# Kernel tuning notes

Hardware: AMD Instinct MI355X
Metric: run time of the kernel (lower is better)

Reference implementation:

```python
import jax, jax.numpy as jnp
import numpy as np

CHUNK = 32
HEADS = 4
EPS_RMS = 1e-5

def silu(x):
    return jax.nn.silu(x)

def l2norm(x, eps=1e-6):
    return x * jax.lax.rsqrt(jnp.sum(x * x, axis=-1, keepdims=True) + eps)

def short_conv(x, w):
    # x: (b, l, c); w: (c, K) depthwise causal conv, no bias
    K = w.shape[1]
    L = x.shape[1]
    xp = jnp.pad(x, ((0, 0), (K - 1, 0), (0, 0)))
    out = xp[:, 0:L, :] * w[:, 0]
    for k in range(1, K):
        out = out + xp[:, k:k + L, :] * w[:, k]
    return out

def delta_rule_chunkwise(q, k, v, beta, chunk=CHUNK):
    # q,k: (b,h,l,dk); v: (b,h,l,dv); beta: (b,h,l). l divisible by chunk.
    b, h, l, dk = q.shape
    dv = v.shape[-1]
    n = l // chunk
    q = l2norm(q)
    k = l2norm(k)
    v = v * beta[..., None]
    k_beta = k * beta[..., None]
    resh = lambda x: x.reshape(b, h, n, chunk, -1)
    q, k, v, k_beta = map(resh, (q, k, v, k_beta))
    strict_lower = jnp.tril(jnp.ones((chunk, chunk), bool), -1)
    # A = -(k_beta k^T) kept strictly lower triangular
    attn = jnp.where(strict_lower, -(k_beta @ jnp.swapaxes(k, -1, -2)), 0.0)
    # forward substitution: T = (I - A)^{-1} - I built row by row (fixed 32 rows)
    for i in range(1, chunk):
        row = attn[..., i, :]                                  # (b,h,n,c)
        new = attn[..., i, :i] + jnp.einsum('...j,...jk->...k', row, attn[..., :, :i])
        attn = attn.at[..., i, :i].set(new)
    attn = attn + jnp.eye(chunk, dtype=attn.dtype)
    u = attn @ v        # (b,h,n,c,dv)
    w = attn @ k_beta   # (b,h,n,c,dk)
    lower_incl = jnp.tril(jnp.ones((chunk, chunk), bool))
    qc, kc, uc, wc = [jnp.moveaxis(x, 2, 0) for x in (q, k, u, w)]
    S0 = jnp.zeros((b, h, dk, dv), q.dtype)
    def step(S, inp):
        q_i, k_i, u_i, w_i = inp
        attn_i = jnp.where(lower_incl, q_i @ jnp.swapaxes(k_i, -1, -2), 0.0)
        u_adj = u_i - w_i @ S
        o_i = q_i @ S + attn_i @ u_adj
        S = S + jnp.swapaxes(k_i, -1, -2) @ u_adj
        return S, o_i
    S, o = jax.lax.scan(step, S0, (qc, kc, uc, wc))
    o = jnp.moveaxis(o, 0, 2).reshape(b, h, l, dv)
    return o, S

def ema_rule(v, gamma):
    # v: (b,h,l,dv), gamma: (b,h,l); sequential EMA scan
    v_t = jnp.moveaxis(v, 2, 0)       # (l,b,h,dv)
    g_t = jnp.moveaxis(gamma, 2, 0)   # (l,b,h)
    s0 = jnp.zeros(v.shape[:2] + (v.shape[-1],), v.dtype)
    def step(s, inp):
        vt, gt = inp
        s = gt[..., None] * s + (1.0 - gt[..., None]) * vt
        return s, s
    s_fin, out = jax.lax.scan(step, s0, (v_t, g_t))
    return jnp.moveaxis(out, 0, 2), s_fin

def rms_norm(x, w, eps=EPS_RMS):
    return x * jax.lax.rsqrt(jnp.mean(x * x, axis=-1, keepdims=True) + eps) * w

def setup_inputs() -> dict:
    key = jax.random.key(0)
    ks = jax.random.split(key, 16)
    b, l, d = 4, 2048, 1024
    H, conv_K = HEADS, 4
    s = 0.02
    return {
        'hidden_states': jax.random.normal(ks[0], (b, l, d), jnp.float32),
        'Wq': jax.random.normal(ks[1], (d, d), jnp.float32) * s,
        'Wk': jax.random.normal(ks[2], (d, d), jnp.float32) * s,
        'Wv': jax.random.normal(ks[3], (d, d), jnp.float32) * s,
        'conv_q': jax.random.normal(ks[4], (d, conv_K), jnp.float32) * 0.3,
        'conv_k': jax.random.normal(ks[5], (d, conv_K), jnp.float32) * 0.3,
        'conv_v': jax.random.normal(ks[6], (d, conv_K), jnp.float32) * 0.3,
        'Wb': jax.random.normal(ks[7], (d, H), jnp.float32) * s,
        'Wdec': jax.random.normal(ks[8], (d, H), jnp.float32) * s,
        'Wmix': jax.random.normal(ks[9], (d, H), jnp.float32) * s,
        'conv_mix': jax.random.normal(ks[10], (H, conv_K), jnp.float32) * 0.3,
        'mix_bias': jnp.full((H,), -2.0, jnp.float32),
        'rms_w': jnp.ones((d // H,), jnp.float32),
        'Wo': jax.random.normal(ks[11], (d, d), jnp.float32) * s,
    }

def reference(hidden_states, Wq, Wk, Wv, conv_q, conv_k, conv_v, Wb, Wdec, Wmix, conv_mix, mix_bias, rms_w, Wo):
    b, l, d = hidden_states.shape
    H = HEADS
    dk = d // H
    dv = d // H
    # projections + causal depthwise short conv (silu activation inside conv)
    q = silu(short_conv(hidden_states @ Wq, conv_q))
    k = silu(short_conv(hidden_states @ Wk, conv_k))
    v = silu(short_conv(hidden_states @ Wv, conv_v))
    mix_inp = silu(short_conv(hidden_states @ Wmix, conv_mix))  # (b,l,H)
    # qk_activation == 'silu' applies an extra silu after conv (per source)
    q = silu(q)
    k = silu(k)
    # split heads -> (b,H,l,dh)
    to_heads = lambda x, dh: jnp.transpose(x.reshape(b, l, H, dh), (0, 2, 1, 3))
    q_d = to_heads(q, dk)
    k_d = to_heads(k, dk)
    v_d = to_heads(v, dv)
    beta = jax.nn.sigmoid(hidden_states @ Wb)           # (b,l,H)
    beta_d = jnp.transpose(beta, (0, 2, 1))             # (b,H,l)
    o_d, S = delta_rule_chunkwise(q_d, k_d, v_d, beta_d)
    o_d = jnp.transpose(o_d, (0, 2, 1, 3))              # (b,l,H,dv)
    # EMA branch
    gamma = jax.nn.sigmoid(hidden_states @ Wdec)        # (b,l,H)
    gamma_d = jnp.transpose(gamma, (0, 2, 1))
    ema_out, ema_state = ema_rule(v_d, gamma_d)
    ema_out = jnp.transpose(ema_out, (0, 2, 1, 3))      # (b,l,H,dv)
    # fine-grained head mix gate
    mix = jax.nn.sigmoid(mix_inp + mix_bias)            # (b,l,H)
    o = (1.0 - mix[..., None]) * o_d + mix[..., None] * ema_out
    # per-head RMSNorm then output projection
    o = rms_norm(o, rms_w)
    out = o.reshape(b, l, H * dv) @ Wo
    return out
```

## Files before the change

### kernel.cpp

```cpp
#include <hip/hip_runtime.h>
#include <hip/hip_bf16.h>

#define B 4
#define L 2048
#define D 1024
#define NH 4
#define DK 256
#define CHUNK 32
#define NCH 64
#define BH (B*NH)
#define ET 64
#define ENCH (L/ET)

typedef __attribute__((ext_vector_type(8))) __bf16 bf16x8;
typedef __attribute__((ext_vector_type(4))) __bf16 bf16x4;
typedef __attribute__((ext_vector_type(4))) float f32x4;

__device__ inline unsigned short f2bf(float f) {
    union { float f; unsigned u; } v; v.f = f;
    unsigned r = v.u + 0x7fffu + ((v.u >> 16) & 1u);
    return (unsigned short)(r >> 16);
}
__device__ inline float bf2f(unsigned short h) {
    union { unsigned u; float f; } v; v.u = ((unsigned)h) << 16; return v.f;
}
__device__ inline float sigmoidf_(float x) { return 1.0f / (1.0f + __expf(-x)); }
__device__ inline float siluf_(float x) { return x / (1.0f + __expf(-x)); }

#define MFMA16(a, b, c) __builtin_amdgcn_mfma_f32_16x16x32_bf16((a), (b), (c), 0, 0, 0)

__device__ inline void bar_lds() {
    __builtin_amdgcn_s_waitcnt(0xC07F);
    __builtin_amdgcn_s_barrier();
}

__device__ inline void load_lds16(const unsigned short* g, unsigned short* l) {
    __builtin_amdgcn_global_load_lds(
        (const __attribute__((address_space(1))) unsigned int*)g,
        (__attribute__((address_space(3))) unsigned int*)l, 16, 0, 0);
}

__global__ __launch_bounds__(256) void k_wT(const float* Wq, const float* Wk, const float* Wv,
                                            const float* Wo, unsigned short* wT)
{
    __shared__ float tile[32][33];
    int z = blockIdx.z;
    const float* W = (z == 0) ? Wq : (z == 1) ? Wk : (z == 2) ? Wv : Wo;
    unsigned short* out = wT + (size_t)z * D * D;
    int kt = blockIdx.x * 32, nt = blockIdx.y * 32;
    int tx = threadIdx.x & 31, ty = threadIdx.x >> 5;
#pragma unroll
    for (int i = 0; i < 4; i++)
        tile[ty + 8 * i][tx] = W[(size_t)(kt + ty + 8 * i) * D + nt + tx];
    __syncthreads();
#pragma unroll
    for (int i = 0; i < 4; i++)
        out[(size_t)(nt + ty + 8 * i) * D + kt + tx] = f2bf(tile[tx][ty + 8 * i]);
}

__global__ __launch_bounds__(256) void k_cvt(const float* h, unsigned short* hb, int n4)
{
    int i = blockIdx.x * blockDim.x + threadIdx.x;
    int stride = gridDim.x * blockDim.x;
    const float4* h4 = (const float4*)h;
    for (; i < n4; i += stride) {
        float4 v = h4[i];
        ushort4 o;
        o.x = f2bf(v.x); o.y = f2bf(v.y); o.z = f2bf(v.z); o.w = f2bf(v.w);
        *(ushort4*)(hb + 4 * (size_t)i) = o;
    }
}

template<int NTOT, bool OUT_F32>
__global__ __launch_bounds__(256) void k_gemm_lds(const unsigned short* __restrict__ A,
                                                  const unsigned short* __restrict__ BT,
                                                  void* __restrict__ outp)
{
    __shared__ __align__(16) unsigned short As[128 * 32];
    __shared__ __align__(16) unsigned short Bs[128 * 32];
    const int K = 1024;
    int tid = threadIdx.x;
    int w = tid >> 6, lane = tid & 63;
    int r16 = lane & 15, quad = lane >> 4;
    int wm = w & 1, wn = w >> 1;
    int bm = blockIdx.x * 128;
    int bn = blockIdx.y * 128;
    int lrow = lane >> 2;
    int lcol = (lane & 3) * 8;
    f32x4 z4 = {0.f, 0.f, 0.f, 0.f};
    f32x4 acc[4][4];
#pragma unroll
    for (int i = 0; i < 4; i++)
#pragma unroll
        for (int j = 0; j < 4; j++) acc[i][j] = z4;

    for (int kt = 0; kt < K; kt += 32) {
#pragma unroll
        for (int j = 0; j < 2; j++) {
            int r0 = (w * 2 + j) * 16;
            load_lds16(A + (size_t)(bm + r0 + lrow) * K + kt + lcol, &As[r0 * 32]);
            load_lds16(BT + (size_t)(bn + r0 + lrow) * K + kt + lcol, &Bs[r0 * 32]);
        }
        __syncthreads();
        bf16x8 af[4], bf[4];
#pragma unroll
        for (int ms = 0; ms < 4; ms++)
            af[ms] = *(const bf16x8*)&As[(wm * 64 + ms * 16 + r16) * 32 + quad * 8];
#pragma unroll
        for (int ns = 0; ns < 4; ns++)
            bf[ns] = *(const bf16x8*)&Bs[(wn * 64 + ns * 16 + r16) * 32 + quad * 8];
#pragma unroll
        for (int ms = 0; ms < 4; ms++)
#pragma unroll
            for (int ns = 0; ns < 4; ns++)
                acc[ms][ns] = MFMA16(af[ms], bf[ns], acc[ms][ns]);
        __syncthreads();
    }
#pragma unroll
    for (int ms = 0; ms < 4; ms++)
#pragma unroll
        for (int ns = 0; ns < 4; ns++)
#pragma unroll
            for (int r = 0; r < 4; r++) {
                int m = bm + wm * 64 + ms * 16 + quad * 4 + r;
                int n = bn + wn * 64 + ns * 16 + r16;
                if (OUT_F32)
                    ((float*)outp)[(size_t)m * NTOT + n] = acc[ms][ns][r];
                else
                    ((unsigned short*)outp)[(size_t)m * NTOT + n] = f2bf(acc[ms][ns][r]);
            }
}

__global__ __launch_bounds__(256) void k_smallproj(const float* hid, const float* Wb, const float* Wd,
                                                   const float* Wm, float* beta, float* gamma, float* xmix)
{
    int wave = threadIdx.x >> 6, lane = threadIdx.x & 63;
    int row = blockIdx.x * 4 + wave;
    const float* hrow = hid + (size_t)row * D;
    float acc[12];
#pragma unroll
    for (int j = 0; j < 12; j++) acc[j] = 0.f;
    for (int i = 0; i < 16; i++) {
        int k = lane + 64 * i;
        float h = hrow[k];
        float4 wb = ((const float4*)Wb)[k];
        float4 wd = ((const float4*)Wd)[k];
        float4 wm = ((const float4*)Wm)[k];
        acc[0] += h * wb.x; acc[1] += h * wb.y; acc[2] += h * wb.z; acc[3] += h * wb.w;
        acc[4] += h * wd.x; acc[5] += h * wd.y; acc[6] += h * wd.z; acc[7] += h * wd.w;
        acc[8] += h * wm.x; acc[9] += h * wm.y; acc[10] += h * wm.z; acc[11] += h * wm.w;
    }
#pragma unroll
    for (int j = 0; j < 12; j++)
        for (int off = 32; off; off >>= 1) acc[j] += __shfl_xor(acc[j], off, 64);
    if (lane < 4) {
        beta[(size_t)row * 4 + lane] = sigmoidf_(acc[lane]);
        gamma[(size_t)row * 4 + lane] = sigmoidf_(acc[4 + lane]);
        xmix[(size_t)row * 4 + lane] = acc[8 + lane];
    }
}

__global__ __launch_bounds__(256) void k_conv(const unsigned short* xqkv,
                                              const float* cq, const float* ck, const float* cv,
                                              float* q, float* k, float* v)
{
    int z = blockIdx.z;
    const float* cw = (z == 0) ? cq : (z == 1) ? ck : cv;
    float* dst = (z == 0) ? q : (z == 1) ? k : v;
    int idx = blockIdx.x * 256 + threadIdx.x;
    int c = idx & (D - 1);
    int t = (idx >> 10) & (L - 1);
    int b = idx >> 21;
    float4 w4 = *(const float4*)(cw + (size_t)c * 4);
    float wv[4] = {w4.x, w4.y, w4.z, w4.w};
    size_t base = ((size_t)(b * L)) * (3 * D) + z * D + c;
    float acc = 0.f;
#pragma unroll
    for (int kk = 0; kk < 4; kk++) {
        int tt = t - 3 + kk;
        if (tt >= 0) acc += wv[kk] * bf2f(xqkv[base + (size_t)tt * (3 * D)]);
    }
    float r = siluf_(acc);
    if (z < 2) r = siluf_(r);
    dst[idx] = r;
}

__global__ __launch_bounds__(256) void k_convmix(const float* xmix, const float* cmix, float* mixinp)
{
    int idx = blockIdx.x * 256 + threadIdx.x;
    int h = idx & 3;
    int t = (idx >> 2) & (L - 1);
    int b = idx >> 13;
    float acc = 0.f;
#pragma unroll
    for (int kk = 0; kk < 4; kk++) {
        int tt = t - 3 + kk;
        if (tt >= 0) acc += cmix[h * 4 + kk] * xmix[((size_t)(b * L + tt) << 2) + h];
    }
    mixinp[idx] = siluf_(acc);
}

__global__ __launch_bounds__(256) void k_l2norm(const float* qbuf, const float* kbuf,
                                                unsigned short* qn, unsigned short* kn)
{
    int wave = threadIdx.x >> 6, lane = threadIdx.x & 63;
    int rid = blockIdx.x * 4 + wave;
    int bh = rid >> 11, t = rid & (L - 1);
    int b = bh >> 2, h = bh & 3;
    size_t src = (size_t)(b * L + t) * D + h * DK + lane * 4;
    float4 q4 = *(const float4*)(qbuf + src);
    float4 k4 = *(const float4*)(kbuf + src);
    float sq = q4.x * q4.x + q4.y * q4.y + q4.z * q4.z + q4.w * q4.w;
    float sk = k4.x * k4.x + k4.y * k4.y + k4.z * k4.z + k4.w * k4.w;
    for (int off = 32; off; off >>= 1) { sq += __shfl_xor(sq, off, 64); sk += __shfl_xor(sk, off, 64); }
    float qsc = rsqrtf(sq + 1e-6f);
    float ksc = rsqrtf(sk + 1e-6f);
    uint2 pq, pk;
    pq.x = f2bf(q4.x * qsc) | ((unsigned)f2bf(q4.y * qsc) << 16);
    pq.y = f2bf(q4.z * qsc) | ((unsigned)f2bf(q4.w * qsc) << 16);
    pk.x = f2bf(k4.x * ksc) | ((unsigned)f2bf(k4.y * ksc) << 16);
    pk.y = f2bf(k4.z * ksc) | ((unsigned)f2bf(k4.w * ksc) << 16);
    *(uint2*)(qn + (size_t)rid * DK + lane * 4) = pq;
    *(uint2*)(kn + (size_t)rid * DK + lane * 4) = pk;
}

#define KTS 40
__global__ __launch_bounds__(256) void k_delta_pre(const unsigned short* qn, const unsigned short* kn,
                                                   const float* vbuf, const float* beta,
                                                   unsigned short* wneg, unsigned short* knT,
                                                   unsigned short* attnb, float* u)
{
    __shared__ __align__(16) unsigned short kTl[256 * KTS];
    __shared__ __align__(16) unsigned short vTl[256 * KTS];
    __shared__ __align__(16) unsigned short T2b[32 * KTS];
    __shared__ float Gs[32 * 33];
    int bx = blockIdx.x;
    int bh = bx >> 6, ch = bx & 63;
    int b = bh >> 2, h = bh & 3;
    int t0 = ch * 32;
    int tid = threadIdx.x;
    int w = tid >> 6, lane = tid & 63;
    int r16 = lane & 15, quad = lane >> 4;
    size_t rowbase = (size_t)(bh * L + t0);
    f32x4 z4 = {0.f, 0.f, 0.f, 0.f};

    if (w < 3) {
        int mi = (w == 0) ? 0 : 1;
        int ni = (w == 2) ? 1 : 0;
        const unsigned short* krm = kn + (rowbase + mi * 16 + r16) * DK;
        const unsigned short* krn = kn + (rowbase + ni * 16 + r16) * DK;
        const unsigned short* qrm = qn + (rowbase + mi * 16 + r16) * DK;
        f32x4 g = z4, qk = z4;
#pragma unroll
        for (int kt = 0; kt < 8; kt++) {
            bf16x8 a  = *(const bf16x8*)(krm + kt * 32 + quad * 8);
            bf16x8 bb = *(const bf16x8*)(krn + kt * 32 + quad * 8);
            bf16x8 qa = *(const bf16x8*)(qrm + kt * 32 + quad * 8);
            g  = MFMA16(a, bb, g);
            qk = MFMA16(qa, bb, qk);
        }
#pragma unroll
        for (int r = 0; r < 4; r++) {
            int i = mi * 16 + quad * 4 + r, j = ni * 16 + r16;
            Gs[i * 33 + j] = g[r];
            attnb[(size_t)(bh * 64 + ch) * 1024 + i * 32 + j] =
                (j <= i) ? f2bf(qk[r]) : (unsigned short)0;
        }
    } else {
#pragma unroll
        for (int r = 0; r < 4; r++) {
            int i = quad * 4 + r, j = 16 + r16;
            attnb[(size_t)(bh * 64 + ch) * 1024 + i * 32 + j] = 0;
        }
    }
    {
        int t = tid & 31, c0 = (tid >> 5) * 32;
        const unsigned short* krow = kn + (rowbase + t) * DK + c0;
        const float* vrow = vbuf + ((size_t)(b * L + t0 + t)) * D + h * DK + c0;
#pragma unroll
        for (int j = 0; j < 32; j += 4) {
            ushort4 kv = *(const ushort4*)(krow + j);
            float4 vv = *(const float4*)(vrow + j);
            kTl[(c0 + j + 0) * KTS + t] = kv.x;
            kTl[(c0 + j + 1) * KTS + t] = kv.y;
            kTl[(c0 + j + 2) * KTS + t] = kv.z;
            kTl[(c0 + j + 3) * KTS + t] = kv.w;
            vTl[(c0 + j + 0) * KTS + t] = f2bf(vv.x);
            vTl[(c0 + j + 1) * KTS + t] = f2bf(vv.y);
            vTl[(c0 + j + 2) * KTS + t] = f2bf(vv.z);
            vTl[(c0 + j + 3) * KTS + t] = f2bf(vv.w);
        }
    }
    __syncthreads();

    if (w == 0) {
        int c = lane & 31;
        float rr[32];
#pragma unroll
        for (int j = 0; j < 32; j++) rr[j] = Gs[j * 33 + c];
        rr[0] = 0.f;
        float bc = beta[(size_t)(b * L + t0 + c) * NH + h];
#pragma unroll
        for (int i = 1; i < 32; i++) {
            float bi = __shfl(bc, i, 64);
            float s = -bi * rr[i];
#pragma unroll
            for (int j = 1; j < i; j++) {
                float aij = -bi * __shfl(rr[i], j, 64);
                s += aij * ((c < j) ? rr[j] : 0.f);
            }
            rr[i] = (c < i) ? s : 0.f;
        }
        if (lane < 32) {
#pragma unroll
            for (int i = 0; i < 32; i++) {
                float val = (rr[i] + ((i == c) ? 1.f : 0.f)) * bc;
                T2b[i * KTS + c] = f2bf(val);
            }
        }
    } else {
        int idx = tid - 64;
        for (int rowc = idx; rowc < 256; rowc += 192) {
            unsigned short* kT = knT + ((size_t)(bh * 64 + ch) * DK + rowc) * 32;
#pragma unroll
            for (int seg = 0; seg < 4; seg++) {
                uint4 d = *(const uint4*)&kTl[rowc * KTS + seg * 8];
                *(uint4*)(kT + seg * 8) = d;
            }
        }
    }
    __syncthreads();

#pragma unroll
    for (int mt = 0; mt < 2; mt++) {
        bf16x8 ta = *(const bf16x8*)&T2b[(mt * 16 + r16) * KTS + quad * 8];
#pragma unroll
        for (int nt2 = 0; nt2 < 4; nt2++) {
            int nt = w * 4 + nt2;
            bf16x8 vb = *(const bf16x8*)&vTl[(nt * 16 + r16) * KTS + quad * 8];
            bf16x8 kb = *(const bf16x8*)&kTl[(nt * 16 + r16) * KTS + quad * 8];
            f32x4 uu = MFMA16(ta, vb, z4);
            f32x4 ww = MFMA16(ta, kb, z4);
            float* ug = u + (rowbase + mt * 16 + quad * 4) * DK + nt * 16 + r16;
            unsigned short* wg = wneg + (rowbase + mt * 16 + quad * 4) * DK + nt * 16 + r16;
#pragma unroll
            for (int r = 0; r < 4; r++) {
                ug[(size_t)r * DK] = uu[r];
                wg[(size_t)r * DK] = f2bf(-ww[r]);
            }
        }
    }
}

__global__ __launch_bounds__(256) void k_ema_local(const float* v, const float* gamma,
                                                   float* ema_local, float* Acum,
                                                   float* s_end, float* Pchunk)
{
    __shared__ float gsh[ET];
    int blk = blockIdx.x;
    int bh = blk >> 5;
    int ch = blk & (ENCH - 1);
    int b = bh >> 2, h = bh & 3;
    int c = threadIdx.x;
    int t0 = ch * ET;
    if (c < ET) gsh[c] = gamma[(size_t)(b * L + t0 + c) * NH + h];
    __syncthreads();
    const float* vg = v + (size_t)(b * L + t0) * D + h * DK + c;
    float* eg = ema_local + (size_t)(b * L + t0) * D + h * DK + c;
    float* Ag = Acum + (size_t)bh * L + t0;
    float s = 0.f;
    float A = 1.f;
#pragma unroll 8
    for (int i = 0; i < ET; i++) {
        float g = gsh[i];
        s = g * s + (1.f - g) * vg[(size_t)i * D];
        A *= g;
        eg[(size_t)i * D] = s;
        if (c == 0) Ag[i] = A;
    }
    s_end[((size_t)bh * ENCH + ch) * DK + c] = s;
    if (c == 0) Pchunk[(size_t)bh * ENCH + ch] = A;
}

__global__ __launch_bounds__(256) void k_ema_carry(const float* s_end, const float* Pchunk, float* S_in)
{
    int bh = blockIdx.x;
    int c = threadIdx.x;
    float S = 0.f;
    for (int ch = 0; ch < ENCH; ch++) {
        S_in[((size_t)bh * ENCH + ch) * DK + c] = S;
        float P = Pchunk[(size_t)bh * ENCH + ch];
        S = P * S + s_end[((size_t)bh * ENCH + ch) * DK + c];
    }
}

#define STS 280
#define USTR 40
__global__ __launch_bounds__(128, 1) void k_scan(const unsigned short* qn, const unsigned short* wneg,
                                                 const unsigned short* knT, const unsigned short* attnb,
                                                 const float* u, float* od)
{
    __shared__ __align__(16) unsigned short st[16 * STS];
    __shared__ __align__(16) unsigned short uat[16 * USTR];
    int bh = blockIdx.x;
    int tile = blockIdx.y;
    int b = bh >> 2, h = bh & 3;
    int mo = threadIdx.x >> 6, lane = threadIdx.x & 63;
    int r16 = lane & 15, quad = lane >> 4;
    int cbase = tile * 16;
    f32x4 z4 = {0.f, 0.f, 0.f, 0.f};
    f32x4 sacc[8];
#pragma unroll
    for (int a = 0; a < 8; a++) sacc[a] = z4;
    const unsigned short* qb = qn + (size_t)bh * L * DK;
    const unsigned short* wb = wneg + (size_t)bh * L * DK;
    const float* ub = u + (size_t)bh * L * DK;
    const unsigned short* kTbase = knT + (size_t)bh * 64 * DK * 32;
    const unsigned short* atbase = attnb + (size_t)bh * 64 * 1024;
    int dkb = mo * 128;

    bf16x8 qf[2][8], wf[2][8];
    f32x4 au0[2];

    auto issue = [&](int ch, int par) {
        int t0 = ch * 32;
        const unsigned short* wrow = wb + (size_t)(t0 + 16 * mo + r16) * DK;
        const unsigned short* qrow = qb + (size_t)(t0 + 16 * mo + r16) * DK;
#pragma unroll
        for (int kt = 0; kt < 8; kt++) {
            qf[par][kt] = *(const bf16x8*)(qrow + kt * 32 + quad * 8);
            wf[par][kt] = *(const bf16x8*)(wrow + kt * 32 + quad * 8);
        }
        const float* up = ub + (size_t)(t0 + 16 * mo + quad * 4) * DK + cbase + r16;
        f32x4 a; a[0] = up[0]; a[1] = up[DK]; a[2] = up[2 * DK]; a[3] = up[3 * DK];
        au0[par] = a;
    };

    issue(0, 0);

    auto body = [&](int ch, int par) {
        int t0 = ch * 32;
        bf16x8 af = *(const bf16x8*)(atbase + (size_t)ch * 1024 + (16 * mo + r16) * 32 + quad * 8);
        const unsigned short* kTb = kTbase + (size_t)ch * DK * 32;
        bf16x8 kf[8];
#pragma unroll
        for (int a = 0; a < 8; a++)
            kf[a] = *(const bf16x8*)(kTb + (size_t)(dkb + a * 16 + r16) * 32 + quad * 8);

#pragma unroll
        for (int a = 0; a < 8; a++) {
            uint2 p;
            p.x = f2bf(sacc[a][0]) | ((unsigned)f2bf(sacc[a][1]) << 16);
            p.y = f2bf(sacc[a][2]) | ((unsigned)f2bf(sacc[a][3]) << 16);
            *(uint2*)&st[r16 * STS + dkb + a * 16 + quad * 4] = p;
        }
        if (ch + 1 < NCH) issue(ch + 1, par ^ 1);
        bar_lds();

        f32x4 au = au0[par], ao = z4;
#pragma unroll
        for (int kt = 0; kt < 8; kt++) {
            bf16x8 sfr = *(const bf16x8*)&st[r16 * STS + kt * 32 + quad * 8];
            au = MFMA16(wf[par][kt], sfr, au);
            ao = MFMA16(qf[par][kt], sfr, ao);
        }
        {
            uint2 p;
            p.x = f2bf(au[0]) | ((unsigned)f2bf(au[1]) << 16);
            p.y = f2bf(au[2]) | ((unsigned)f2bf(au[3]) << 16);
            *(uint2*)&uat[r16 * USTR + 16 * mo + quad * 4] = p;
        }
        bar_lds();

        {
            bf16x8 uf = *(const bf16x8*)&uat[r16 * USTR + quad * 8];
            ao = MFMA16(af, uf, ao);
            float* op = od + (size_t)(b * L + t0 + 16 * mo + quad * 4) * D + h * DK + cbase + r16;
            op[0] = ao[0]; op[D] = ao[1]; op[2 * D] = ao[2]; op[3 * D] = ao[3];
#pragma unroll
            for (int a = 0; a < 8; a++)
                sacc[a] = MFMA16(kf[a], uf, sacc[a]);
        }
    };

    for (int ch2 = 0; ch2 < NCH; ch2 += 2) {
        body(ch2, 0);
        body(ch2 + 1, 1);
    }
}

__global__ __launch_bounds__(256) void k_mixrms(const float* od, const float* ema_local,
                                                const float* Acum, const float* S_in,
                                                const float* mixinp,
                                                const float* mix_bias, const float* rms_w,
                                                unsigned short* onorm)
{
    int row = blockIdx.x;
    int tid = threadIdx.x;
    int h = tid >> 6, lane = tid & 63;
    int b = row >> 11, t = row & (L - 1);
    int bh = b * NH + h;
    int ch = t >> 6;
    float m = sigmoidf_(mixinp[(size_t)row * NH + h] + mix_bias[h]);
    int c = tid * 4;
    float A = Acum[(size_t)bh * L + t];
    float4 sin4 = *(const float4*)(S_in + ((size_t)bh * ENCH + ch) * DK + (c & (DK - 1)));
    float4 o = *(const float4*)(od + (size_t)row * D + c);
    float4 e = *(const float4*)(ema_local + (size_t)row * D + c);
    e.x += A * sin4.x; e.y += A * sin4.y; e.z += A * sin4.z; e.w += A * sin4.w;
    float x0 = o.x + m * (e.x - o.x);
    float x1 = o.y + m * (e.y - o.y);
    float x2 = o.z + m * (e.z - o.z);
    float x3 = o.w + m * (e.w - o.w);
    float ss = x0 * x0 + x1 * x1 + x2 * x2 + x3 * x3;
    for (int off = 32; off; off >>= 1) ss += __shfl_xor(ss, off, 64);
    float scale = rsqrtf(ss * (1.0f / 256.0f) + 1e-5f);
    float4 w = *(const float4*)(rms_w + lane * 4);
    uint2 p;
    p.x = f2bf(x0 * scale * w.x) | ((unsigned)f2bf(x1 * scale * w.y) << 16);
    p.y = f2bf(x2 * scale * w.z) | ((unsigned)f2bf(x3 * scale * w.w) << 16);
    *(uint2*)(onorm + (size_t)row * D + c) = p;
}

extern "C" void kernel_launch(void* const* d_in, const int* in_sizes, int n_in,
                              void* d_out, int out_size, void* d_ws, size_t ws_size,
                              hipStream_t stream)
{
    (void)in_sizes; (void)n_in; (void)out_size; (void)ws_size;
    const float* hidden   = (const float*)d_in[0];
    const float* Wq       = (const float*)d_in[1];
    const float* Wk       = (const float*)d_in[2];
    const float* Wv       = (const float*)d_in[3];
    const float* conv_q   = (const float*)d_in[4];
    const float* conv_k   = (const float*)d_in[5];
    const float* conv_v   = (const float*)d_in[6];
    const float* Wb       = (const float*)d_in[7];
    const float* Wdec     = (const float*)d_in[8];
    const float* Wmix     = (const float*)d_in[9];
    const float* conv_mix = (const float*)d_in[10];
    const float* mix_bias = (const float*)d_in[11];
    const float* rms_w    = (const float*)d_in[12];
    const float* Wo       = (const float*)d_in[13];
    float* out = (float*)d_out;

    char* ws = (char*)d_ws;
    size_t off = 0;
    auto alloc = [&](size_t bytes) -> char* {
        char* p = ws + off;
        off += (bytes + 255) & ~(size_t)255;
        return p;
    };
    unsigned short* wT    = (unsigned short*)alloc((size_t)4 * D * D * 2);
    unsigned short* hidB  = (unsigned short*)alloc((size_t)B * L * D * 2);
    unsigned short* xqkv  = (unsigned short*)alloc((size_t)B * L * 3 * D * 2);
    float* beta   = (float*)alloc((size_t)B * L * NH * 4);
    float* gamma  = (float*)alloc((size_t)B * L * NH * 4);
    float* xmix   = (float*)alloc((size_t)B * L * NH * 4);
    float* mixinp = (float*)alloc((size_t)B * L * NH * 4);
    float* qbuf   = (float*)alloc((size_t)B * L * D * 4);
    float* kbuf   = (float*)alloc((size_t)B * L * D * 4);
    float* vbuf   = (float*)alloc((size_t)B * L * D * 4);
    float* u      = (float*)alloc((size_t)B * L * D * 4);
    unsigned short* attnb = (unsigned short*)alloc((size_t)BH * NCH * CHUNK * CHUNK * 2);
    unsigned short* onorm = (unsigned short*)alloc((size_t)B * L * D * 2);
    unsigned short* kn    = (unsigned short*)alloc((size_t)B * L * D * 2);
    float* Acum   = (float*)alloc((size_t)BH * L * 4);
    float* s_end  = (float*)alloc((size_t)BH * ENCH * DK * 4);
    float* Pchunk = (float*)alloc((size_t)BH * ENCH * 4);
    float* S_in   = (float*)alloc((size_t)BH * ENCH * DK * 4);

    unsigned short* qn   = xqkv;
    unsigned short* wneg = xqkv + (size_t)B * L * D;
    unsigned short* knT  = xqkv + (size_t)2 * B * L * D;
    float* ema_local = qbuf;
    float* od  = kbuf;

    k_wT<<<dim3(32, 32, 4), 256, 0, stream>>>(Wq, Wk, Wv, Wo, wT);
    k_cvt<<<dim3(2048), 256, 0, stream>>>(hidden, hidB, B * L * D / 4);
    k_gemm_lds<3 * D, false><<<dim3(64, 24), 256, 0, stream>>>(hidB, wT, xqkv);
    k_smallproj<<<dim3(B * L / 4), 256, 0, stream>>>(hidden, Wb, Wdec, Wmix, beta, gamma, xmix);
    k_conv<<<dim3(B * L * D / 256, 1, 3), 256, 0, stream>>>(xqkv, conv_q, conv_k, conv_v,
                                                            qbuf, kbuf, vbuf);
    k_convmix<<<dim3(B * L * NH / 256), 256, 0, stream>>>(xmix, conv_mix, mixinp);
    k_l2norm<<<dim3(BH * L / 4), 256, 0, stream>>>(qbuf, kbuf, qn, kn);
    k_delta_pre<<<dim3(BH * NCH), 256, 0, stream>>>(qn, kn, vbuf, beta, wneg, knT, attnb, u);
    k_ema_local<<<dim3(BH * ENCH), 256, 0, stream>>>(vbuf, gamma, ema_local, Acum, s_end, Pchunk);
    k_ema_carry<<<dim3(BH), 256, 0, stream>>>(s_end, Pchunk, S_in);
    k_scan<<<dim3(16, 16), 128, 0, stream>>>(qn, wneg, knT, attnb, u, od);
    k_mixrms<<<dim3(B * L), 256, 0, stream>>>(od, ema_local, Acum, S_in, mixinp, mix_bias, rms_w, onorm);
    k_gemm_lds<D, true><<<dim3(64, 8), 256, 0, stream>>>(onorm, wT + (size_t)3 * D * D, out);
}
```

Baseline: 517.0 us.

## Fuse short conv, SiLU and L2 norm into one kernel with bf16 v

```diff
diff --git a/kernel.cpp b/kernel.cpp
--- a/kernel.cpp
+++ b/kernel.cpp
@@ -160,29 +160,65 @@
     }
 }
 
-__global__ __launch_bounds__(256) void k_conv(const unsigned short* xqkv,
-                                              const float* cq, const float* ck, const float* cv,
-                                              float* q, float* k, float* v)
-{
-    int z = blockIdx.z;
-    const float* cw = (z == 0) ? cq : (z == 1) ? ck : cv;
-    float* dst = (z == 0) ? q : (z == 1) ? k : v;
-    int idx = blockIdx.x * 256 + threadIdx.x;
-    int c = idx & (D - 1);
-    int t = (idx >> 10) & (L - 1);
-    int b = idx >> 21;
-    float4 w4 = *(const float4*)(cw + (size_t)c * 4);
-    float wv[4] = {w4.x, w4.y, w4.z, w4.w};
-    size_t base = ((size_t)(b * L)) * (3 * D) + z * D + c;
-    float acc = 0.f;
+__global__ __launch_bounds__(256) void k_convnorm(const unsigned short* __restrict__ xqkv,
+                                                  const float* __restrict__ cq,
+                                                  const float* __restrict__ ck,
+                                                  const float* __restrict__ cv,
+                                                  unsigned short* __restrict__ qn,
+                                                  unsigned short* __restrict__ kn,
+                                                  unsigned short* __restrict__ vb)
+{
+    int row = blockIdx.x;
+    int t = row & (L - 1);
+    int b = row >> 11;
+    int tid = threadIdx.x;
+    int h = tid >> 6, lane = tid & 63;
+    int c = tid * 4;
+    float wq[4][4], wk[4][4], wv[4][4];
+#pragma unroll
+    for (int j = 0; j < 4; j++) {
+        float4 a = *(const float4*)(cq + (size_t)(c + j) * 4);
+        wq[j][0] = a.x; wq[j][1] = a.y; wq[j][2] = a.z; wq[j][3] = a.w;
+        float4 d = *(const float4*)(ck + (size_t)(c + j) * 4);
+        wk[j][0] = d.x; wk[j][1] = d.y; wk[j][2] = d.z; wk[j][3] = d.w;
+        float4 e = *(const float4*)(cv + (size_t)(c + j) * 4);
+        wv[j][0] = e.x; wv[j][1] = e.y; wv[j][2] = e.z; wv[j][3] = e.w;
+    }
+    float aq[4] = {0, 0, 0, 0}, ak[4] = {0, 0, 0, 0}, av[4] = {0, 0, 0, 0};
 #pragma unroll
     for (int kk = 0; kk < 4; kk++) {
         int tt = t - 3 + kk;
-        if (tt >= 0) acc += wv[kk] * bf2f(xqkv[base + (size_t)tt * (3 * D)]);
-    }
-    float r = siluf_(acc);
-    if (z < 2) r = siluf_(r);
-    dst[idx] = r;
+        if (tt < 0) continue;
+        const unsigned short* p = xqkv + (size_t)(row - 3 + kk) * (3 * D) + c;
+        ushort4 xq = *(const ushort4*)(p);
+        ushort4 xk = *(const ushort4*)(p + D);
+        ushort4 xv = *(const ushort4*)(p + 2 * D);
+        aq[0] += wq[0][kk] * bf2f(xq.x); aq[1] += wq[1][kk] * bf2f(xq.y);
+        aq[2] += wq[2][kk] * bf2f(xq.z); aq[3] += wq[3][kk] * bf2f(xq.w);
+        ak[0] += wk[0][kk] * bf2f(xk.x); ak[1] += wk[1][kk] * bf2f(xk.y);
+        ak[2] += wk[2][kk] * bf2f(xk.z); ak[3] += wk[3][kk] * bf2f(xk.w);
+        av[0] += wv[0][kk] * bf2f(xv.x); av[1] += wv[1][kk] * bf2f(xv.y);
+        av[2] += wv[2][kk] * bf2f(xv.z); av[3] += wv[3][kk] * bf2f(xv.w);
+    }
+    float rq[4], rk[4], rv[4];
+#pragma unroll
+    for (int j = 0; j < 4; j++) {
+        rq[j] = siluf_(siluf_(aq[j]));
+        rk[j] = siluf_(siluf_(ak[j]));
+        rv[j] = siluf_(av[j]);
+    }
+    float sq = rq[0] * rq[0] + rq[1] * rq[1] + rq[2] * rq[2] + rq[3] * rq[3];
+    float sk = rk[0] * rk[0] + rk[1] * rk[1] + rk[2] * rk[2] + rk[3] * rk[3];
+    for (int off = 32; off; off >>= 1) { sq += __shfl_xor(sq, off, 64); sk += __shfl_xor(sk, off, 64); }
+    float qs = rsqrtf(sq + 1e-6f), ks = rsqrtf(sk + 1e-6f);
+    size_t oidx = ((size_t)(b * NH + h) * L + t) * DK + lane * 4;
+    ushort4 oq, ok, ov;
+    oq.x = f2bf(rq[0] * qs); oq.y = f2bf(rq[1] * qs); oq.z = f2bf(rq[2] * qs); oq.w = f2bf(rq[3] * qs);
+    ok.x = f2bf(rk[0] * ks); ok.y = f2bf(rk[1] * ks); ok.z = f2bf(rk[2] * ks); ok.w = f2bf(rk[3] * ks);
+    ov.x = f2bf(rv[0]); ov.y = f2bf(rv[1]); ov.z = f2bf(rv[2]); ov.w = f2bf(rv[3]);
+    *(ushort4*)(qn + oidx) = oq;
+    *(ushort4*)(kn + oidx) = ok;
+    *(ushort4*)(vb + (size_t)row * D + c) = ov;
 }
 
 __global__ __launch_bounds__(256) void k_convmix(const float* xmix, const float* cmix, float* mixinp)
@@ -200,33 +236,9 @@
     mixinp[idx] = siluf_(acc);
 }
 
-__global__ __launch_bounds__(256) void k_l2norm(const float* qbuf, const float* kbuf,
-                                                unsigned short* qn, unsigned short* kn)
-{
-    int wave = threadIdx.x >> 6, lane = threadIdx.x & 63;
-    int rid = blockIdx.x * 4 + wave;
-    int bh = rid >> 11, t = rid & (L - 1);
-    int b = bh >> 2, h = bh & 3;
-    size_t src = (size_t)(b * L + t) * D + h * DK + lane * 4;
-    float4 q4 = *(const float4*)(qbuf + src);
-    float4 k4 = *(const float4*)(kbuf + src);
-    float sq = q4.x * q4.x + q4.y * q4.y + q4.z * q4.z + q4.w * q4.w;
-    float sk = k4.x * k4.x + k4.y * k4.y + k4.z * k4.z + k4.w * k4.w;
-    for (int off = 32; off; off >>= 1) { sq += __shfl_xor(sq, off, 64); sk += __shfl_xor(sk, off, 64); }
-    float qsc = rsqrtf(sq + 1e-6f);
-    float ksc = rsqrtf(sk + 1e-6f);
-    uint2 pq, pk;
-    pq.x = f2bf(q4.x * qsc) | ((unsigned)f2bf(q4.y * qsc) << 16);
-    pq.y = f2bf(q4.z * qsc) | ((unsigned)f2bf(q4.w * qsc) << 16);
-    pk.x = f2bf(k4.x * ksc) | ((unsigned)f2bf(k4.y * ksc) << 16);
-    pk.y = f2bf(k4.z * ksc) | ((unsigned)f2bf(k4.w * ksc) << 16);
-    *(uint2*)(qn + (size_t)rid * DK + lane * 4) = pq;
-    *(uint2*)(kn + (size_t)rid * DK + lane * 4) = pk;
-}
-
 #define KTS 40
 __global__ __launch_bounds__(256) void k_delta_pre(const unsigned short* qn, const unsigned short* kn,
-                                                   const float* vbuf, const float* beta,
+                                                   const unsigned short* vb, const float* beta,
                                                    unsigned short* wneg, unsigned short* knT,
                                                    unsigned short* attnb, float* u)
 {
@@ -276,19 +288,19 @@
     {
         int t = tid & 31, c0 = (tid >> 5) * 32;
         const unsigned short* krow = kn + (rowbase + t) * DK + c0;
-        const float* vrow = vbuf + ((size_t)(b * L + t0 + t)) * D + h * DK + c0;
+        const unsigned short* vrow = vb + ((size_t)(b * L + t0 + t)) * D + h * DK + c0;
 #pragma unroll
         for (int j = 0; j < 32; j += 4) {
             ushort4 kv = *(const ushort4*)(krow + j);
-            float4 vv = *(const float4*)(vrow + j);
+            ushort4 vv = *(const ushort4*)(vrow + j);
             kTl[(c0 + j + 0) * KTS + t] = kv.x;
             kTl[(c0 + j + 1) * KTS + t] = kv.y;
             kTl[(c0 + j + 2) * KTS + t] = kv.z;
             kTl[(c0 + j + 3) * KTS + t] = kv.w;
-            vTl[(c0 + j + 0) * KTS + t] = f2bf(vv.x);
-            vTl[(c0 + j + 1) * KTS + t] = f2bf(vv.y);
-            vTl[(c0 + j + 2) * KTS + t] = f2bf(vv.z);
-            vTl[(c0 + j + 3) * KTS + t] = f2bf(vv.w);
+            vTl[(c0 + j + 0) * KTS + t] = vv.x;
+            vTl[(c0 + j + 1) * KTS + t] = vv.y;
+            vTl[(c0 + j + 2) * KTS + t] = vv.z;
+            vTl[(c0 + j + 3) * KTS + t] = vv.w;
         }
     }
     __syncthreads();
@@ -337,9 +349,9 @@
 #pragma unroll
         for (int nt2 = 0; nt2 < 4; nt2++) {
             int nt = w * 4 + nt2;
-            bf16x8 vb = *(const bf16x8*)&vTl[(nt * 16 + r16) * KTS + quad * 8];
+            bf16x8 vb2 = *(const bf16x8*)&vTl[(nt * 16 + r16) * KTS + quad * 8];
             bf16x8 kb = *(const bf16x8*)&kTl[(nt * 16 + r16) * KTS + quad * 8];
-            f32x4 uu = MFMA16(ta, vb, z4);
+            f32x4 uu = MFMA16(ta, vb2, z4);
             f32x4 ww = MFMA16(ta, kb, z4);
             float* ug = u + (rowbase + mt * 16 + quad * 4) * DK + nt * 16 + r16;
             unsigned short* wg = wneg + (rowbase + mt * 16 + quad * 4) * DK + nt * 16 + r16;
@@ -352,7 +364,7 @@
     }
 }
 
-__global__ __launch_bounds__(256) void k_ema_local(const float* v, const float* gamma,
+__global__ __launch_bounds__(256) void k_ema_local(const unsigned short* v, const float* gamma,
                                                    float* ema_local, float* Acum,
                                                    float* s_end, float* Pchunk)
 {
@@ -365,7 +377,7 @@
     int t0 = ch * ET;
     if (c < ET) gsh[c] = gamma[(size_t)(b * L + t0 + c) * NH + h];
     __syncthreads();
-    const float* vg = v + (size_t)(b * L + t0) * D + h * DK + c;
+    const unsigned short* vg = v + (size_t)(b * L + t0) * D + h * DK + c;
     float* eg = ema_local + (size_t)(b * L + t0) * D + h * DK + c;
     float* Ag = Acum + (size_t)bh * L + t0;
     float s = 0.f;
@@ -373,7 +385,7 @@
 #pragma unroll 8
     for (int i = 0; i < ET; i++) {
         float g = gsh[i];
-        s = g * s + (1.f - g) * vg[(size_t)i * D];
+        s = g * s + (1.f - g) * bf2f(vg[(size_t)i * D]);
         A *= g;
         eg[(size_t)i * D] = s;
         if (c == 0) Ag[i] = A;
@@ -559,17 +571,17 @@
     float* mixinp = (float*)alloc((size_t)B * L * NH * 4);
     float* qbuf   = (float*)alloc((size_t)B * L * D * 4);
     float* kbuf   = (float*)alloc((size_t)B * L * D * 4);
-    float* vbuf   = (float*)alloc((size_t)B * L * D * 4);
+    unsigned short* vb = (unsigned short*)alloc((size_t)B * L * D * 2);
     float* u      = (float*)alloc((size_t)B * L * D * 4);
     unsigned short* attnb = (unsigned short*)alloc((size_t)BH * NCH * CHUNK * CHUNK * 2);
     unsigned short* onorm = (unsigned short*)alloc((size_t)B * L * D * 2);
     unsigned short* kn    = (unsigned short*)alloc((size_t)B * L * D * 2);
+    unsigned short* qn    = (unsigned short*)alloc((size_t)B * L * D * 2);
     float* Acum   = (float*)alloc((size_t)BH * L * 4);
     float* s_end  = (float*)alloc((size_t)BH * ENCH * DK * 4);
     float* Pchunk = (float*)alloc((size_t)BH * ENCH * 4);
     float* S_in   = (float*)alloc((size_t)BH * ENCH * DK * 4);
 
-    unsigned short* qn   = xqkv;
     unsigned short* wneg = xqkv + (size_t)B * L * D;
     unsigned short* knT  = xqkv + (size_t)2 * B * L * D;
     float* ema_local = qbuf;
@@ -579,12 +591,10 @@
     k_cvt<<<dim3(2048), 256, 0, stream>>>(hidden, hidB, B * L * D / 4);
     k_gemm_lds<3 * D, false><<<dim3(64, 24), 256, 0, stream>>>(hidB, wT, xqkv);
     k_smallproj<<<dim3(B * L / 4), 256, 0, stream>>>(hidden, Wb, Wdec, Wmix, beta, gamma, xmix);
-    k_conv<<<dim3(B * L * D / 256, 1, 3), 256, 0, stream>>>(xqkv, conv_q, conv_k, conv_v,
-                                                            qbuf, kbuf, vbuf);
+    k_convnorm<<<dim3(B * L), 256, 0, stream>>>(xqkv, conv_q, conv_k, conv_v, qn, kn, vb);
     k_convmix<<<dim3(B * L * NH / 256), 256, 0, stream>>>(xmix, conv_mix, mixinp);
-    k_l2norm<<<dim3(BH * L / 4), 256, 0, stream>>>(qbuf, kbuf, qn, kn);
-    k_delta_pre<<<dim3(BH * NCH), 256, 0, stream>>>(qn, kn, vbuf, beta, wneg, knT, attnb, u);
-    k_ema_local<<<dim3(BH * ENCH), 256, 0, stream>>>(vbuf, gamma, ema_local, Acum, s_end, Pchunk);
+    k_delta_pre<<<dim3(BH * NCH), 256, 0, stream>>>(qn, kn, vb, beta, wneg, knT, attnb, u);
+    k_ema_local<<<dim3(BH * ENCH), 256, 0, stream>>>(vb, gamma, ema_local, Acum, s_end, Pchunk);
     k_ema_carry<<<dim3(BH), 256, 0, stream>>>(s_end, Pchunk, S_in);
     k_scan<<<dim3(16, 16), 128, 0, stream>>>(qn, wneg, knT, attnb, u, od);
     k_mixrms<<<dim3(B * L), 256, 0, stream>>>(od, ema_local, Acum, S_in, mixinp, mix_bias, rms_w, onorm);
```

After: 496.5 us. 4.0% less time.
